# Kernel tuning notes

Measured on AMD Instinct MI355X. Metric: run time of the kernel, lower is better.

## Reference

```python
import jax, jax.numpy as jnp
import numpy as np

V, D, T, B, MS, WIN, EOS = 10000, 256, 128, 8, 4, 1, 4
S = MS + 1          # decoder segment length (y_input0 + MAX_SEGMENT tokens)
HRATE = 0.1
LOGINF = 1e6


def setup_inputs() -> dict:
    key = jax.random.key(0)
    ks = jax.random.split(key, 17)
    s = lambda i, shape: (jax.random.normal(ks[i], shape, jnp.float32) * 0.05)
    return dict(
        x_ids=jax.random.randint(ks[0], (B, T + 2 * WIN), 0, V),
        lens=jnp.full((B,), T, dtype=jnp.int32),
        emb=s(1, (V, D)),
        y_start=s(2, (1, D)),
        cell_Wi=s(3, (4 * D, D)), cell_Wh=s(4, (4 * D, D)), cell_b=s(5, (4 * D,)),
        yin0_W=s(6, (D, D)), yin0_b=s(7, (D,)),
        hlin_W=s(8, (2 * D, D)), hlin_b=s(9, (2 * D,)),
        l0_Wi=s(10, (4 * D, D)), l0_Wh=s(11, (4 * D, D)), l0_b=s(12, (4 * D,)),
        l1_Wi=s(13, (4 * D, D)), l1_Wh=s(14, (4 * D, D)), l1_b=s(15, (4 * D,)),
        out_b=s(16, (V,)),
    )


def _cell(x, h, c, Wi, Wh, b):
    # torch LSTM gate order: i, f, g, o
    g = x @ Wi.T + h @ Wh.T + b
    i, f, gg, o = jnp.split(g, 4, axis=-1)
    c2 = jax.nn.sigmoid(f) * c + jax.nn.sigmoid(i) * jnp.tanh(gg)
    return jax.nn.sigmoid(o) * jnp.tanh(c2), c2


def reference(x_ids, lens, emb, y_start, cell_Wi, cell_Wh, cell_b,
              yin0_W, yin0_b, hlin_W, hlin_b,
              l0_Wi, l0_Wh, l0_b, l1_Wi, l1_Wh, l1_b, out_b):
    y = x_ids[:, WIN:-WIN]                     # [B, T] target ids
    x = emb[y]                                 # [B, T, D]

    # --- encoder LSTMCell scan over j_start (state persists across schedule) ---
    seq = jnp.concatenate(
        [jnp.broadcast_to(y_start, (B, D))[None], jnp.transpose(x, (1, 0, 2))[:-1]], 0)  # [T,B,D]
    z = jnp.zeros((B, D), x.dtype)
    def enc_step(carry, xt):
        h, c = carry
        h2, c2 = _cell(xt, h, c, cell_Wi, cell_Wh, cell_b)
        return (h2, c2), h2
    _, h_seq = jax.lax.scan(enc_step, (z, z), seq)        # [T, B, D]

    drop_h = HRATE * h_seq
    y_in0 = drop_h @ yin0_W.T + yin0_b                    # [T, B, D]
    h0_all = jnp.tanh(drop_h @ hlin_W.T + hlin_b).reshape(T, B, 2, D)  # per-layer init h

    # --- build decoder inputs [T, B, S, D]: (y_input0, x[j_start:j_start+MS]) ---
    xp = jnp.pad(x, ((0, 0), (0, MS), (0, 0)))            # zero-pad time (causal => pads don't affect valid outputs)
    pos = jnp.arange(T)[:, None] + jnp.arange(MS)[None, :]           # [T, MS]
    seg_x = jnp.transpose(xp[:, pos], (1, 0, 2, 3))       # [T, B, MS, D]
    seg = jnp.concatenate([y_in0[:, :, None, :], seg_x], axis=2)     # [T, B, S, D]

    # --- 2-layer LSTM decoder, vmapped over j_start ---
    def decode(seg_t, h_init):                            # seg_t [B,S,D], h_init [B,2,D]
        def step(carry, xt):
            (h0, c0), (h1, c1) = carry
            h0n, c0n = _cell(xt, h0, c0, l0_Wi, l0_Wh, l0_b)
            h1n, c1n = _cell(h0n, h1, c1, l1_Wi, l1_Wh, l1_b)
            return ((h0n, c0n), (h1n, c1n)), h1n
        init = ((h_init[:, 0], z), (h_init[:, 1], z))
        _, hs = jax.lax.scan(step, init, jnp.transpose(seg_t, (1, 0, 2)))
        return jnp.transpose(hs, (1, 0, 2))               # [B, S, D]
    dec_h = jax.vmap(decode)(seg, h0_all)                 # [T, B, S, D]

    # --- tied output projection + log-softmax (only needed gathers kept) ---
    logits = jnp.einsum('tbsd,vd->tbsv', dec_h, emb) + out_b         # [T,B,S,V]
    logZ = jax.nn.logsumexp(logits, axis=-1)                          # [T,B,S]

    tgt = jnp.transpose(y[:, jnp.clip(pos, 0, T - 1)], (1, 0, 2))     # [T,B,MS]
    tgt_lp = jnp.take_along_axis(logits[:, :, :MS, :], tgt[..., None], axis=3)[..., 0] \
             - logZ[:, :, :MS]                                        # [T,B,MS]
    pmask = (pos < T)[:, None, :]
    cum = jnp.cumsum(jnp.where(pmask, tgt_lp, 0.0), axis=2)           # [T,B,MS]
    eos_lp = logits[:, :, 1:, EOS] - logZ[:, :, 1:]                   # [T,B,MS]

    kmask = (jnp.arange(T)[:, None] + jnp.arange(1, MS + 1)[None, :]) <= T   # [T,MS]
    body = jnp.where(kmask[:, None, :], cum + eos_lp, -LOGINF)        # [T,B,MS]
    logpy = jnp.concatenate([jnp.full((T, 1, B), -LOGINF, body.dtype),
                             jnp.transpose(body, (0, 2, 1))], axis=1)  # [T, MS+1, B]

    # --- alpha forward DP: alpha[j] = logsumexp_L alpha[j-L] + logpy[j-L][L] ---
    jj = jnp.arange(1, T + 1)[:, None]
    ii = jnp.arange(MS)[None, :]
    sstart = jj - MS + ii                                             # [T,MS]
    LPG = jnp.where((sstart >= 0)[..., None],
                    logpy[jnp.clip(sstart, 0), jnp.broadcast_to(MS - ii, (T, MS))],
                    -LOGINF)                                          # [T,MS,B]

    Apad0 = jnp.full((MS + T + 1, B), -LOGINF, logpy.dtype).at[MS].set(0.0)
    def dp_step(Apad, args):
        j, lpg = args
        win = jax.lax.dynamic_slice(Apad, (j, 0), (MS, B))            # alpha[j-MS .. j-1]
        aj = jax.nn.logsumexp(win + lpg, axis=0)
        return jax.lax.dynamic_update_slice(Apad, aj[None], (MS + j, 0)), None
    Apad, _ = jax.lax.scan(dp_step, Apad0, (jnp.arange(1, T + 1), LPG))
    alpha = Apad[MS:]                                                 # [T+1, B]

    ret = -jnp.sum(alpha[lens, jnp.arange(B)]) / jnp.sum(lens).astype(alpha.dtype)
    return ret
```

## Files before the change

### kernel.cpp

```cpp
#include <hip/hip_runtime.h>

#define V_ 10000
#define D_ 256
#define T_ 128
#define B_ 8
#define MS_ 4
#define S_ 5
#define EOS_ 4

typedef unsigned short b16_t;
typedef __attribute__((ext_vector_type(8))) short s16x8;
typedef __attribute__((ext_vector_type(8))) unsigned short u16x8;
typedef __attribute__((ext_vector_type(4))) float f32x4;
typedef __attribute__((ext_vector_type(2))) _Float16 h16x2;

__device__ inline b16_t f2bf(float f) {
  union { float f; unsigned u; } v; v.f = f;
  unsigned r = v.u + 0x7FFFu + ((v.u >> 16) & 1u);
  return (b16_t)(r >> 16);
}
__device__ inline float bf2f(b16_t h) {
  union { unsigned u; float f; } v; v.u = ((unsigned)h) << 16; return v.f;
}
__device__ inline float sigm_(float x) { return 1.0f / (1.0f + __expf(-x)); }
__device__ inline float tanh_(float x) { return 2.0f / (1.0f + __expf(-2.0f * x)) - 1.0f; }
__device__ inline h16x2 bch(unsigned u) { return __builtin_bit_cast(h16x2, u); }
__device__ inline unsigned pkh(float a, float b) {
  h16x2 v; v.x = (_Float16)a; v.y = (_Float16)b;
  return __builtin_bit_cast(unsigned, v);
}

#if __has_builtin(__builtin_amdgcn_fdot2)
#define FDOT2(a, b, c) __builtin_amdgcn_fdot2((a), (b), (c), false)
#else
#define FDOT2(a, b, c) ((c) + (float)(a).x * (float)(b).x + (float)(a).y * (float)(b).y)
#endif

__device__ inline void cvt4(const float* __restrict__ s, b16_t* __restrict__ d) {
  float4 v = *(const float4*)s;
  ushort4 o = { f2bf(v.x), f2bf(v.y), f2bf(v.z), f2bf(v.w) };
  *(ushort4*)d = o;
}

__global__ void k_prep(const float* __restrict__ emb, const float* __restrict__ cWi,
                       const float* __restrict__ y0W, const float* __restrict__ hlW,
                       const float* __restrict__ l0Wi, const float* __restrict__ l0Wh,
                       const float* __restrict__ l1Wi, const float* __restrict__ l1Wh,
                       const float* __restrict__ cWh, const int* __restrict__ x_ids,
                       const float* __restrict__ y_st,
                       b16_t* __restrict__ emb_bf, b16_t* __restrict__ cWi_bf,
                       b16_t* __restrict__ y0W_bf, b16_t* __restrict__ hlW_bf,
                       b16_t* __restrict__ l0Wi_bf, b16_t* __restrict__ l0Wh_bf,
                       b16_t* __restrict__ Wcat_bf, unsigned* __restrict__ Whf,
                       b16_t* __restrict__ seq_bf, b16_t* __restrict__ seg_bf) {
  for (long i = (long)blockIdx.x * blockDim.x + threadIdx.x; i < 1410048L;
       i += (long)gridDim.x * blockDim.x) {
    if (i < 640000L) { cvt4(emb + i * 4, emb_bf + i * 4); }
    else if (i < 705536L) { long j = i - 640000L; cvt4(cWi + j * 4, cWi_bf + j * 4); }
    else if (i < 721920L) { long j = i - 705536L; cvt4(y0W + j * 4, y0W_bf + j * 4); }
    else if (i < 754688L) { long j = i - 721920L; cvt4(hlW + j * 4, hlW_bf + j * 4); }
    else if (i < 820224L) { long j = i - 754688L; cvt4(l0Wi + j * 4, l0Wi_bf + j * 4); }
    else if (i < 885760L) { long j = i - 820224L; cvt4(l0Wh + j * 4, l0Wh_bf + j * 4); }
    else if (i < 1016832L) {
      long j = (i - 885760L) * 4;
      long n = j >> 9; int k = (int)(j & 511);
      const float* src = (k < 256) ? (l1Wi + n * 256 + k) : (l1Wh + n * 256 + (k - 256));
      cvt4(src, Wcat_bf + j);
    } else if (i < 1082368L) {
      long j = i - 1016832L;
      float4 v = *(const float4*)(cWh + j * 4);
      Whf[2 * j] = pkh(v.x, v.y);
      Whf[2 * j + 1] = pkh(v.z, v.w);
    } else if (i < 1147904L) {
      long j = i - 1082368L;
      int m = (int)(j >> 6), c = (int)(j & 63) * 4;
      int t = m >> 3, b = m & 7;
      const float* src = (t == 0) ? (y_st + c)
                                  : (emb + (size_t)x_ids[b * (T_ + 2) + t] * D_ + c);
      cvt4(src, seq_bf + (size_t)m * D_ + c);
    } else {
      long j = i - 1147904L;
      int r = (int)(j >> 6), c = (int)(j & 63) * 4;
      int p = r >> 2, s = 1 + (r & 3);
      int t = p >> 3, b = p & 7;
      int tt = t + s - 1;
      int ps = r + (r >> 2) + 1;
      if (tt < T_) {
        int tok = x_ids[b * (T_ + 2) + tt + 1];
        cvt4(emb + (size_t)tok * D_ + c, seg_bf + (size_t)ps * 256 + c);
      } else {
        ushort4 z = {0, 0, 0, 0};
        *(ushort4*)(seg_bf + (size_t)ps * 256 + c) = z;
      }
    }
  }
}

__global__ __launch_bounds__(256) void k_gemm_big(
    const b16_t* __restrict__ seq_bf, const b16_t* __restrict__ cWi_bf,
    const float* __restrict__ cb, float* __restrict__ encX,
    const b16_t* __restrict__ seg_bf, const b16_t* __restrict__ l0Wi_bf,
    const float* __restrict__ l0b, float* __restrict__ X0) {
  __shared__ b16_t As[64][264];
  __shared__ b16_t Bs[64][264];
  int bx = blockIdx.x, by = blockIdx.y;
  const b16_t* Ab; const b16_t* Bw; const float* bias; float* C;
  int rb, remap;
  if (bx < 16) { Ab = seq_bf; Bw = cWi_bf; bias = cb; C = encX; rb = bx * 64; remap = 0; }
  else { Ab = seg_bf; Bw = l0Wi_bf; bias = l0b; C = X0; rb = (bx - 16) * 64; remap = 1; }
  int colBase = by * 64;
  int tid = threadIdx.x;
  for (int i = tid; i < 64 * 32; i += 256) {
    int r = i >> 5, c = (i & 31) * 8;
    int rr = rb + r;
    int ar = remap ? (rr + (rr >> 2) + 1) : rr;
    *(u16x8*)&As[r][c] = *(const u16x8*)(Ab + (size_t)ar * 256 + c);
    *(u16x8*)&Bs[r][c] = *(const u16x8*)(Bw + (size_t)(colBase + r) * 256 + c);
  }
  __syncthreads();
  int w = tid >> 6, l = tid & 63, lr = l & 15, kg = l >> 4;
  f32x4 acc[4] = {{0.f,0.f,0.f,0.f},{0.f,0.f,0.f,0.f},{0.f,0.f,0.f,0.f},{0.f,0.f,0.f,0.f}};
  for (int kk = 0; kk < 8; ++kk) {
    s16x8 a = *(const s16x8*)&As[w * 16 + lr][kk * 32 + kg * 8];
#pragma unroll
    for (int f = 0; f < 4; ++f) {
      s16x8 b = *(const s16x8*)&Bs[f * 16 + lr][kk * 32 + kg * 8];
      acc[f] = __builtin_amdgcn_mfma_f32_16x16x32_bf16(a, b, acc[f], 0, 0, 0);
    }
  }
#pragma unroll
  for (int f = 0; f < 4; ++f) {
#pragma unroll
    for (int r = 0; r < 4; ++r) {
      int mm = rb + w * 16 + kg * 4 + r;
      int cr = remap ? (mm + (mm >> 2) + 1) : mm;
      int n = colBase + f * 16 + lr;
      C[(size_t)cr * 1024 + n] = acc[f][r] + bias[n];
    }
  }
}

__global__ __launch_bounds__(512) __attribute__((amdgpu_waves_per_eu(2, 2)))
void k_encoder(const unsigned* __restrict__ Whf, const float* __restrict__ encX,
               b16_t* __restrict__ droph) {
  __shared__ uint4 wtail[16][512];
  __shared__ unsigned hbuf[128];
  __shared__ float gl[1024];
  int batch = blockIdx.x;
  int tid = threadIdx.x;
  int r0 = tid, r1 = tid + 512;
  unsigned wa[96], wb[96];
  {
    const uint4* p0 = (const uint4*)(Whf + (size_t)r0 * 128);
    const uint4* p1 = (const uint4*)(Whf + (size_t)r1 * 128);
#pragma unroll
    for (int i = 0; i < 24; ++i) {
      uint4 v = p0[i];
      wa[4*i] = v.x; wa[4*i+1] = v.y; wa[4*i+2] = v.z; wa[4*i+3] = v.w;
    }
#pragma unroll
    for (int i = 0; i < 24; ++i) {
      uint4 v = p1[i];
      wb[4*i] = v.x; wb[4*i+1] = v.y; wb[4*i+2] = v.z; wb[4*i+3] = v.w;
    }
#pragma unroll
    for (int i = 0; i < 8; ++i) wtail[i][tid] = p0[24 + i];
#pragma unroll
    for (int i = 0; i < 8; ++i) wtail[8 + i][tid] = p1[24 + i];
  }
#pragma unroll
  for (int i = 0; i < 96; ++i) asm volatile("v_mov_b32 %0, %0" : "+v"(wa[i]));
#pragma unroll
  for (int i = 0; i < 96; ++i) asm volatile("v_mov_b32 %0, %0" : "+v"(wb[i]));
  if (tid < 128) hbuf[tid] = 0;
  float c = 0.f;
  float a0n = encX[((size_t)0 * 8 + batch) * 1024 + r0];
  float a1n = encX[((size_t)0 * 8 + batch) * 1024 + r1];
  __syncthreads();
#pragma unroll 1
  for (int t = 0; t < 128; ++t) {
    float a0 = a0n, a1 = a1n;
    if (t < 127) {
      a0n = encX[((size_t)(t + 1) * 8 + batch) * 1024 + r0];
      a1n = encX[((size_t)(t + 1) * 8 + batch) * 1024 + r1];
    }
    float s0 = 0.f, s1 = 0.f, s2 = 0.f, s3 = 0.f;
#pragma unroll
    for (int j = 0; j < 24; ++j) {
      uint4 hv = *(const uint4*)&hbuf[4 * j];
      s0 = FDOT2(bch(hv.x), bch(wa[4*j+0]), s0);
      s0 = FDOT2(bch(hv.y), bch(wa[4*j+1]), s0);
      s1 = FDOT2(bch(hv.z), bch(wa[4*j+2]), s1);
      s1 = FDOT2(bch(hv.w), bch(wa[4*j+3]), s1);
      s2 = FDOT2(bch(hv.x), bch(wb[4*j+0]), s2);
      s2 = FDOT2(bch(hv.y), bch(wb[4*j+1]), s2);
      s3 = FDOT2(bch(hv.z), bch(wb[4*j+2]), s3);
      s3 = FDOT2(bch(hv.w), bch(wb[4*j+3]), s3);
    }
#pragma unroll
    for (int j = 0; j < 8; ++j) {
      uint4 hv = *(const uint4*)&hbuf[96 + 4 * j];
      uint4 w0 = wtail[j][tid];
      uint4 w1 = wtail[8 + j][tid];
      s0 = FDOT2(bch(hv.x), bch(w0.x), s0);
      s0 = FDOT2(bch(hv.y), bch(w0.y), s0);
      s1 = FDOT2(bch(hv.z), bch(w0.z), s1);
      s1 = FDOT2(bch(hv.w), bch(w0.w), s1);
      s2 = FDOT2(bch(hv.x), bch(w1.x), s2);
      s2 = FDOT2(bch(hv.y), bch(w1.y), s2);
      s3 = FDOT2(bch(hv.z), bch(w1.z), s3);
      s3 = FDOT2(bch(hv.w), bch(w1.w), s3);
    }
    gl[r0] = a0 + s0 + s1;
    gl[r1] = a1 + s2 + s3;
    __syncthreads();
    if (tid < 256) {
      float gi = gl[tid],       gf = gl[256 + tid];
      float gg = gl[512 + tid], go = gl[768 + tid];
      float c2 = sigm_(gf) * c + sigm_(gi) * tanh_(gg);
      float h2 = sigm_(go) * tanh_(c2);
      c = c2;
      droph[((size_t)t * 8 + batch) * 256 + tid] = f2bf(0.1f * h2);
      ((_Float16*)hbuf)[tid] = (_Float16)h2;
    }
    __syncthreads();
  }
}

__global__ __launch_bounds__(256) void k_proj(
    const b16_t* __restrict__ droph, const b16_t* __restrict__ y0W_bf,
    const float* __restrict__ y0b, const b16_t* __restrict__ hlW_bf,
    const float* __restrict__ hlb, b16_t* __restrict__ seg_bf,
    b16_t* __restrict__ hcat) {
  __shared__ b16_t As[64][264];
  __shared__ b16_t Bs[64][264];
  int bx = blockIdx.x, by = blockIdx.y;
  const b16_t* Bw; const float* bias; int colBase, mode;
  if (by < 4) { Bw = y0W_bf; bias = y0b; colBase = by * 64; mode = 0; }
  else { Bw = hlW_bf; bias = hlb; colBase = (by - 4) * 64; mode = 1; }
  int rowBase = bx * 64;
  int tid = threadIdx.x;
  for (int i = tid; i < 64 * 32; i += 256) {
    int r = i >> 5, c = (i & 31) * 8;
    *(u16x8*)&As[r][c] = *(const u16x8*)(droph + (size_t)(rowBase + r) * 256 + c);
    *(u16x8*)&Bs[r][c] = *(const u16x8*)(Bw + (size_t)(colBase + r) * 256 + c);
  }
  __syncthreads();
  int w = tid >> 6, l = tid & 63, lr = l & 15, kg = l >> 4;
  f32x4 acc[4] = {{0.f,0.f,0.f,0.f},{0.f,0.f,0.f,0.f},{0.f,0.f,0.f,0.f},{0.f,0.f,0.f,0.f}};
  for (int kk = 0; kk < 8; ++kk) {
    s16x8 a = *(const s16x8*)&As[w * 16 + lr][kk * 32 + kg * 8];
#pragma unroll
    for (int f = 0; f < 4; ++f) {
      s16x8 b = *(const s16x8*)&Bs[f * 16 + lr][kk * 32 + kg * 8];
      acc[f] = __builtin_amdgcn_mfma_f32_16x16x32_bf16(a, b, acc[f], 0, 0, 0);
    }
  }
#pragma unroll
  for (int f = 0; f < 4; ++f) {
#pragma unroll
    for (int r = 0; r < 4; ++r) {
      int m = rowBase + w * 16 + kg * 4 + r;
      int n = colBase + f * 16 + lr;
      float v = acc[f][r] + bias[n];
      if (mode == 0) seg_bf[(size_t)m * 1280 + n] = f2bf(v);
      else hcat[(size_t)m * 512 + n] = f2bf(tanh_(v));
    }
  }
}

__global__ __launch_bounds__(256) void k_gemm(const b16_t* __restrict__ A, int lda,
                                              const b16_t* __restrict__ Bw,
                                              const float* __restrict__ bias,
                                              float* __restrict__ C, int ldc) {
  __shared__ b16_t As[64][264];
  __shared__ b16_t Bs[64][264];
  int tid = threadIdx.x;
  int rowBase = blockIdx.x * 64, colBase = blockIdx.y * 64;
  for (int i = tid; i < 64 * 32; i += 256) {
    int r = i >> 5, c = (i & 31) * 8;
    *(u16x8*)&As[r][c] = *(const u16x8*)(A + (size_t)(rowBase + r) * lda + c);
    *(u16x8*)&Bs[r][c] = *(const u16x8*)(Bw + (size_t)(colBase + r) * 256 + c);
  }
  __syncthreads();
  int w = tid >> 6, l = tid & 63, lr = l & 15, kg = l >> 4;
  f32x4 acc[4] = {{0.f,0.f,0.f,0.f},{0.f,0.f,0.f,0.f},{0.f,0.f,0.f,0.f},{0.f,0.f,0.f,0.f}};
  for (int kk = 0; kk < 8; ++kk) {
    s16x8 a = *(const s16x8*)&As[w * 16 + lr][kk * 32 + kg * 8];
#pragma unroll
    for (int f = 0; f < 4; ++f) {
      s16x8 b = *(const s16x8*)&Bs[f * 16 + lr][kk * 32 + kg * 8];
      acc[f] = __builtin_amdgcn_mfma_f32_16x16x32_bf16(a, b, acc[f], 0, 0, 0);
    }
  }
#pragma unroll
  for (int f = 0; f < 4; ++f) {
#pragma unroll
    for (int r = 0; r < 4; ++r) {
      int m = rowBase + w * 16 + kg * 4 + r;
      int n = colBase + f * 16 + lr;
      C[(size_t)m * ldc + n] = acc[f][r] + bias[n];
    }
  }
}

__global__ __launch_bounds__(512) void k_dec2(
    b16_t* __restrict__ hcat,
    const b16_t* __restrict__ l0Wh_bf,
    const b16_t* __restrict__ Wcat_bf,
    const float* __restrict__ X0,
    const float* __restrict__ l1b,
    float* __restrict__ c0, float* __restrict__ c1,
    b16_t* __restrict__ dec_out, int s) {
  __shared__ b16_t A0s[16][264];
  __shared__ b16_t A1s[16][520];
  int tid = threadIdx.x;
  int R0 = blockIdx.x * 16;
  for (int i = tid; i < 16 * 32; i += 512) {
    int r = i >> 5, cc = (i & 31) * 8;
    *(u16x8*)&A0s[r][cc] = *(const u16x8*)(hcat + (size_t)(R0 + r) * 512 + cc);
    *(u16x8*)&A1s[r][256 + cc] = *(const u16x8*)(hcat + (size_t)(R0 + r) * 512 + 256 + cc);
  }
  __syncthreads();
  int w = tid >> 6, l = tid & 63, lr = l & 15, kg = l >> 4;
  {
    s16x8 af[8];
#pragma unroll
    for (int kk = 0; kk < 8; ++kk)
      af[kk] = *(const s16x8*)&A0s[lr][kk * 32 + kg * 8];
    f32x4 acc[4][2];
#pragma unroll
    for (int g = 0; g < 4; ++g)
#pragma unroll
      for (int ct = 0; ct < 2; ++ct) acc[g][ct] = f32x4{0.f, 0.f, 0.f, 0.f};
#pragma unroll
    for (int g = 0; g < 4; ++g)
#pragma unroll
      for (int ct = 0; ct < 2; ++ct) {
        int n = g * 256 + w * 32 + ct * 16 + lr;
        const b16_t* bp = l0Wh_bf + (size_t)n * 256 + kg * 8;
#pragma unroll
        for (int kk = 0; kk < 8; ++kk)
          acc[g][ct] = __builtin_amdgcn_mfma_f32_16x16x32_bf16(
              af[kk], *(const s16x8*)(bp + kk * 32), acc[g][ct], 0, 0, 0);
      }
#pragma unroll
    for (int ct = 0; ct < 2; ++ct)
#pragma unroll
      for (int r = 0; r < 4; ++r) {
        int row = kg * 4 + r, p = R0 + row, d = w * 32 + ct * 16 + lr;
        const float* xp = X0 + ((size_t)p * 5 + s) * 1024;
        float gi = acc[0][ct][r] + xp[d],       gf = acc[1][ct][r] + xp[256 + d];
        float gg = acc[2][ct][r] + xp[512 + d], go = acc[3][ct][r] + xp[768 + d];
        float cc0 = c0[(size_t)p * 256 + d];
        float c2 = sigm_(gf) * cc0 + sigm_(gi) * tanh_(gg);
        float h2 = sigm_(go) * tanh_(c2);
        c0[(size_t)p * 256 + d] = c2;
        b16_t hb = f2bf(h2);
        A1s[row][d] = hb;
        hcat[(size_t)p * 512 + d] = hb;
      }
  }
  __syncthreads();
  {
    s16x8 a1[16];
#pragma unroll
    for (int kk = 0; kk < 16; ++kk)
      a1[kk] = *(const s16x8*)&A1s[lr][kk * 32 + kg * 8];
    f32x4 acc[4][2];
#pragma unroll
    for (int g = 0; g < 4; ++g)
#pragma unroll
      for (int ct = 0; ct < 2; ++ct) acc[g][ct] = f32x4{0.f, 0.f, 0.f, 0.f};
#pragma unroll
    for (int g = 0; g < 4; ++g)
#pragma unroll
      for (int ct = 0; ct < 2; ++ct) {
        int n = g * 256 + w * 32 + ct * 16 + lr;
        const b16_t* bp = Wcat_bf + (size_t)n * 512 + kg * 8;
#pragma unroll
        for (int kk = 0; kk < 16; ++kk)
          acc[g][ct] = __builtin_amdgcn_mfma_f32_16x16x32_bf16(
              a1[kk], *(const s16x8*)(bp + kk * 32), acc[g][ct], 0, 0, 0);
      }
#pragma unroll
    for (int ct = 0; ct < 2; ++ct)
#pragma unroll
      for (int r = 0; r < 4; ++r) {
        int row = kg * 4 + r, p = R0 + row, d = w * 32 + ct * 16 + lr;
        float gi = acc[0][ct][r] + l1b[d],       gf = acc[1][ct][r] + l1b[256 + d];
        float gg = acc[2][ct][r] + l1b[512 + d], go = acc[3][ct][r] + l1b[768 + d];
        float cc1 = c1[(size_t)p * 256 + d];
        float c2 = sigm_(gf) * cc1 + sigm_(gi) * tanh_(gg);
        float h2 = sigm_(go) * tanh_(c2);
        c1[(size_t)p * 256 + d] = c2;
        b16_t hb = f2bf(h2);
        hcat[(size_t)p * 512 + 256 + d] = hb;
        dec_out[((size_t)p * 5 + s) * 256 + d] = hb;
      }
  }
}

__global__ __launch_bounds__(512) void k_logits(const b16_t* __restrict__ Abf,
                                                const b16_t* __restrict__ emb_bf,
                                                const float* __restrict__ out_b,
                                                float* __restrict__ sumexp) {
  __shared__ b16_t Bs[64][264];
  int tid = threadIdx.x;
  int rowBase = blockIdx.x * 128;
  int w = tid >> 6, l = tid & 63, lr = l & 15, kg = l >> 4;
  s16x8 af[8];
  {
    const b16_t* arow = Abf + (size_t)(rowBase + w * 16 + lr) * 256;
#pragma unroll
    for (int kk = 0; kk < 8; ++kk) af[kk] = *(const s16x8*)(arow + kk * 32 + kg * 8);
  }
  float runsum[4] = {0.f, 0.f, 0.f, 0.f};
  int t0 = blockIdx.y * 12, t1 = (t0 + 12 < 157) ? (t0 + 12) : 157;
  for (int tile = t0; tile < t1; ++tile) {
    int colBase = tile * 64;
    __syncthreads();
    for (int i = tid; i < 64 * 32; i += 512) {
      int r = i >> 5, cc = (i & 31) * 8;
      int vrow = colBase + r;
      u16x8 bv = {0, 0, 0, 0, 0, 0, 0, 0};
      if (vrow < V_) bv = *(const u16x8*)(emb_bf + (size_t)vrow * D_ + cc);
      *(u16x8*)&Bs[r][cc] = bv;
    }
    __syncthreads();
    f32x4 acc[4] = {{0.f,0.f,0.f,0.f},{0.f,0.f,0.f,0.f},{0.f,0.f,0.f,0.f},{0.f,0.f,0.f,0.f}};
#pragma unroll
    for (int kk = 0; kk < 8; ++kk) {
#pragma unroll
      for (int f = 0; f < 4; ++f) {
        s16x8 b = *(const s16x8*)&Bs[f * 16 + lr][kk * 32 + kg * 8];
        acc[f] = __builtin_amdgcn_mfma_f32_16x16x32_bf16(af[kk], b, acc[f], 0, 0, 0);
      }
    }
#pragma unroll
    for (int f = 0; f < 4; ++f) {
      int n = colBase + f * 16 + lr;
      if (n < V_) {
        float ob = out_b[n];
#pragma unroll
        for (int r = 0; r < 4; ++r) runsum[r] += __expf(acc[f][r] + ob);
      }
    }
  }
#pragma unroll
  for (int r = 0; r < 4; ++r) {
    float rs = runsum[r];
    rs += __shfl_xor(rs, 1, 64);
    rs += __shfl_xor(rs, 2, 64);
    rs += __shfl_xor(rs, 4, 64);
    rs += __shfl_xor(rs, 8, 64);
    if (lr == 0) atomicAdd(&sumexp[rowBase + w * 16 + kg * 4 + r], rs);
  }
}

__global__ void k_extract(const b16_t* __restrict__ dec_h, const b16_t* __restrict__ emb_bf,
                          const float* __restrict__ out_b, const int* __restrict__ x_ids,
                          float* __restrict__ tl, float* __restrict__ el) {
  int p = blockIdx.x, lane = threadIdx.x;
  int t = p >> 3, b = p & 7;
  for (int s = 0; s < S_; ++s) {
    const b16_t* hr = dec_h + ((size_t)p * S_ + s) * D_;
    float hv[4];
#pragma unroll
    for (int j = 0; j < 4; ++j) hv[j] = bf2f(hr[lane * 4 + j]);
    if (s < MS_) {
      int pos = t + s; if (pos > T_ - 1) pos = T_ - 1;
      int tok = x_ids[b * (T_ + 2) + pos + 1];
      const b16_t* er = emb_bf + (size_t)tok * D_;
      float ps = 0.f;
#pragma unroll
      for (int j = 0; j < 4; ++j) ps += hv[j] * bf2f(er[lane * 4 + j]);
      for (int m = 1; m < 64; m <<= 1) ps += __shfl_xor(ps, m, 64);
      if (lane == 0) tl[p * MS_ + s] = ps + out_b[tok];
    }
    if (s >= 1) {
      const b16_t* er = emb_bf + (size_t)EOS_ * D_;
      float ps = 0.f;
#pragma unroll
      for (int j = 0; j < 4; ++j) ps += hv[j] * bf2f(er[lane * 4 + j]);
      for (int m = 1; m < 64; m <<= 1) ps += __shfl_xor(ps, m, 64);
      if (lane == 0) el[p * MS_ + (s - 1)] = ps + out_b[EOS_];
    }
  }
}

__global__ __launch_bounds__(256) void k_final(const float* __restrict__ sumexp,
                                               const float* __restrict__ tl,
                                               const float* __restrict__ el,
                                               const int* __restrict__ lens,
                                               float* __restrict__ out) {
  __shared__ float logpy[T_][S_][B_];
  __shared__ float alpha[T_ + 1][B_];
  int tid = threadIdx.x;
  for (int p = tid; p < T_ * B_; p += 256) {
    int t = p >> 3, b = p & 7;
    float lz[S_];
#pragma unroll
    for (int s = 0; s < S_; ++s) lz[s] = __logf(sumexp[p * S_ + s]);
    float cum = 0.f, cums[MS_];
#pragma unroll
    for (int s = 0; s < MS_; ++s) {
      float tlp = tl[p * MS_ + s] - lz[s];
      if (t + s < T_) cum += tlp;
      cums[s] = cum;
    }
#pragma unroll
    for (int k = 1; k <= MS_; ++k) {
      float bv = -1000000.0f;
      if (t + k <= T_) bv = cums[k - 1] + (el[p * MS_ + (k - 1)] - lz[k]);
      logpy[t][k][b] = bv;
    }
  }
  __syncthreads();
  if (tid < B_) {
    int b = tid;
    alpha[0][b] = 0.f;
    for (int j = 1; j <= T_; ++j) {
      float vs[MS_], vmax = -1e30f;
#pragma unroll
      for (int k = 1; k <= MS_; ++k) {
        float vv = -2000000.0f;
        if (j - k >= 0) vv = alpha[j - k][b] + logpy[j - k][k][b];
        vs[k - 1] = vv;
        if (vv > vmax) vmax = vv;
      }
      float ssum = 0.f;
#pragma unroll
      for (int k = 0; k < MS_; ++k) ssum += __expf(vs[k] - vmax);
      alpha[j][b] = vmax + __logf(ssum);
    }
  }
  __syncthreads();
  if (tid == 0) {
    float num = 0.f, den = 0.f;
    for (int b = 0; b < B_; ++b) { num += alpha[lens[b]][b]; den += (float)lens[b]; }
    out[0] = -num / den;
  }
}

extern "C" void kernel_launch(void* const* d_in, const int* in_sizes, int n_in,
                              void* d_out, int out_size, void* d_ws, size_t ws_size,
                              hipStream_t stream) {
  const int* x_ids   = (const int*)d_in[0];
  const int* lens    = (const int*)d_in[1];
  const float* emb   = (const float*)d_in[2];
  const float* y_st  = (const float*)d_in[3];
  const float* cWi   = (const float*)d_in[4];
  const float* cWh   = (const float*)d_in[5];
  const float* cb    = (const float*)d_in[6];
  const float* y0W   = (const float*)d_in[7];
  const float* y0b   = (const float*)d_in[8];
  const float* hlW   = (const float*)d_in[9];
  const float* hlb   = (const float*)d_in[10];
  const float* l0Wi  = (const float*)d_in[11];
  const float* l0Wh  = (const float*)d_in[12];
  const float* l0b   = (const float*)d_in[13];
  const float* l1Wi  = (const float*)d_in[14];
  const float* l1Wh  = (const float*)d_in[15];
  const float* l1b   = (const float*)d_in[16];
  const float* outb  = (const float*)d_in[17];
  float* out = (float*)d_out;
  (void)in_sizes; (void)n_in; (void)out_size; (void)ws_size;

  char* ws = (char*)d_ws;
  size_t cur = 0;
  auto alloc = [&](size_t bytes) { size_t o = cur; cur += (bytes + 255) & ~(size_t)255; return o; };
  b16_t* emb_bf    = (b16_t*)(ws + alloc((size_t)V_ * D_ * 2));
  b16_t* cWi_bf    = (b16_t*)(ws + alloc(1024 * 256 * 2));
  b16_t* y0W_bf    = (b16_t*)(ws + alloc(256 * 256 * 2));
  b16_t* hlW_bf    = (b16_t*)(ws + alloc(512 * 256 * 2));
  b16_t* l0Wi_bf   = (b16_t*)(ws + alloc(1024 * 256 * 2));
  b16_t* l0Wh_bf   = (b16_t*)(ws + alloc(1024 * 256 * 2));
  b16_t* Wcat_bf   = (b16_t*)(ws + alloc(1024 * 512 * 2));
  unsigned* Whf    = (unsigned*)(ws + alloc(1024 * 128 * 4));
  b16_t* seq_bf    = (b16_t*)(ws + alloc(1024 * 256 * 2));
  float* encX      = (float*)(ws + alloc((size_t)1024 * 1024 * 4));
  b16_t* droph_bf  = (b16_t*)(ws + alloc(1024 * 256 * 2));
  b16_t* hcat      = (b16_t*)(ws + alloc(1024 * 512 * 2));
  b16_t* seg_bf    = (b16_t*)(ws + alloc((size_t)5120 * 256 * 2));
  float* X0        = (float*)(ws + alloc((size_t)5120 * 1024 * 4));
  float* c0        = (float*)(ws + alloc((size_t)2 * 1024 * 256 * 4));
  float* c1        = c0 + 1024 * 256;
  b16_t* dec_h_bf  = (b16_t*)(ws + alloc((size_t)5120 * 256 * 2));
  float* sumexp    = (float*)(ws + alloc(5120 * 4));
  float* tl        = (float*)(ws + alloc(1024 * MS_ * 4));
  float* el        = (float*)(ws + alloc(1024 * MS_ * 4));

  hipMemsetAsync(sumexp, 0, 5120 * 4, stream);
  hipMemsetAsync(c0, 0, (size_t)2 * 1024 * 256 * 4, stream);

  k_prep<<<1024, 256, 0, stream>>>(emb, cWi, y0W, hlW, l0Wi, l0Wh, l1Wi, l1Wh, cWh,
                                   x_ids, y_st,
                                   emb_bf, cWi_bf, y0W_bf, hlW_bf, l0Wi_bf, l0Wh_bf,
                                   Wcat_bf, Whf, seq_bf, seg_bf);

  k_gemm_big<<<dim3(80, 16), 256, 0, stream>>>(seq_bf, cWi_bf, cb, encX,
                                               seg_bf, l0Wi_bf, l0b, X0);
  k_encoder<<<8, 512, 0, stream>>>(Whf, encX, droph_bf);

  k_proj<<<dim3(16, 12), 256, 0, stream>>>(droph_bf, y0W_bf, y0b, hlW_bf, hlb,
                                           seg_bf, hcat);
  k_gemm<<<dim3(16, 16), 256, 0, stream>>>(seg_bf, 1280, l0Wi_bf, l0b, X0, 5120);

  for (int s = 0; s < S_; ++s)
    k_dec2<<<64, 512, 0, stream>>>(hcat, l0Wh_bf, Wcat_bf, X0, l1b, c0, c1, dec_h_bf, s);

  k_logits<<<dim3(40, 14), 512, 0, stream>>>(dec_h_bf, emb_bf, outb, sumexp);
  k_extract<<<1024, 64, 0, stream>>>(dec_h_bf, emb_bf, outb, x_ids, tl, el);
  k_final<<<1, 256, 0, stream>>>(sumexp, tl, el, lens, out);
}
```

Measured before the change: 657.3 us.

## Fuse decoder steps into one kernel and restructure encoder recurrent matvec

The five per-step decoder launches become one kernel that loops over segment positions. Cell states are kept in registers and hidden states in shared memory instead of round-tripping through global memory, which also removes the cell-state memset. The encoder recurrence is rewritten so each group of four lanes splits one row's K dimension, reducing partial sums with DPP quad swaps. All weights are held in VGPRs and AGPRs, with the h buffer padded per quarter to avoid LDS bank conflicts. This removes launch overhead and global state traffic, at the cost of high register pressure and extra cross-lane shuffles in the serial encoder loop.

```diff
diff --git a/kernel.cpp b/kernel.cpp
--- a/kernel.cpp
+++ b/kernel.cpp
@@ -35,6 +35,15 @@
 #else
 #define FDOT2(a, b, c) ((c) + (float)(a).x * (float)(b).x + (float)(a).y * (float)(b).y)
 #endif
+
+__device__ inline float qswap1(float x) {
+  return __builtin_bit_cast(float, __builtin_amdgcn_update_dpp(
+      0, __builtin_bit_cast(int, x), 0xB1, 0xF, 0xF, true));
+}
+__device__ inline float qswap2(float x) {
+  return __builtin_bit_cast(float, __builtin_amdgcn_update_dpp(
+      0, __builtin_bit_cast(int, x), 0x4E, 0xF, 0xF, true));
+}
 
 __device__ inline void cvt4(const float* __restrict__ s, b16_t* __restrict__ d) {
   float4 v = *(const float4*)s;
@@ -140,88 +149,92 @@
   }
 }
 
-__global__ __launch_bounds__(512) __attribute__((amdgpu_waves_per_eu(2, 2)))
-void k_encoder(const unsigned* __restrict__ Whf, const float* __restrict__ encX,
-               b16_t* __restrict__ droph) {
-  __shared__ uint4 wtail[16][512];
-  __shared__ unsigned hbuf[128];
+__global__ __launch_bounds__(512, 2) void k_encoder(
+    const unsigned* __restrict__ Whf, const float* __restrict__ encX,
+    b16_t* __restrict__ droph) {
+  __shared__ unsigned hbuf[144];
   __shared__ float gl[1024];
   int batch = blockIdx.x;
   int tid = threadIdx.x;
-  int r0 = tid, r1 = tid + 512;
-  unsigned wa[96], wb[96];
-  {
-    const uint4* p0 = (const uint4*)(Whf + (size_t)r0 * 128);
-    const uint4* p1 = (const uint4*)(Whf + (size_t)r1 * 128);
-#pragma unroll
-    for (int i = 0; i < 24; ++i) {
-      uint4 v = p0[i];
-      wa[4*i] = v.x; wa[4*i+1] = v.y; wa[4*i+2] = v.z; wa[4*i+3] = v.w;
-    }
-#pragma unroll
-    for (int i = 0; i < 24; ++i) {
-      uint4 v = p1[i];
-      wb[4*i] = v.x; wb[4*i+1] = v.y; wb[4*i+2] = v.z; wb[4*i+3] = v.w;
-    }
-#pragma unroll
-    for (int i = 0; i < 8; ++i) wtail[i][tid] = p0[24 + i];
-#pragma unroll
-    for (int i = 0; i < 8; ++i) wtail[8 + i][tid] = p1[24 + i];
-  }
-#pragma unroll
-  for (int i = 0; i < 96; ++i) asm volatile("v_mov_b32 %0, %0" : "+v"(wa[i]));
-#pragma unroll
-  for (int i = 0; i < 96; ++i) asm volatile("v_mov_b32 %0, %0" : "+v"(wb[i]));
-  if (tid < 128) hbuf[tid] = 0;
+  int lane = tid & 63;
+  int q = lane & 3;
+  int slot = (tid >> 6) * 16 + (lane >> 2);
+  int r0 = slot * 8;
+  unsigned wv_[160], wa_[96];
+#pragma unroll
+  for (int j = 0; j < 5; ++j) {
+    const uint4* p = (const uint4*)(Whf + (size_t)(r0 + j) * 128 + q * 32);
+#pragma unroll
+    for (int i = 0; i < 8; ++i) {
+      uint4 v = p[i];
+      wv_[j*32+4*i] = v.x; wv_[j*32+4*i+1] = v.y; wv_[j*32+4*i+2] = v.z; wv_[j*32+4*i+3] = v.w;
+    }
+  }
+#pragma unroll
+  for (int j = 0; j < 3; ++j) {
+    const uint4* p = (const uint4*)(Whf + (size_t)(r0 + 5 + j) * 128 + q * 32);
+#pragma unroll
+    for (int i = 0; i < 8; ++i) {
+      uint4 v = p[i];
+      wa_[j*32+4*i] = v.x; wa_[j*32+4*i+1] = v.y; wa_[j*32+4*i+2] = v.z; wa_[j*32+4*i+3] = v.w;
+    }
+  }
+#pragma unroll
+  for (int i = 0; i < 160; ++i) asm volatile("" : "+v"(wv_[i]));
+#pragma unroll
+  for (int i = 0; i < 96; ++i) asm volatile("" : "+a"(wa_[i]));
+  if (tid < 144) hbuf[tid] = 0;
   float c = 0.f;
-  float a0n = encX[((size_t)0 * 8 + batch) * 1024 + r0];
-  float a1n = encX[((size_t)0 * 8 + batch) * 1024 + r1];
+  float exa = encX[(size_t)batch * 1024 + r0 + q];
+  float exb = encX[(size_t)batch * 1024 + r0 + 4 + q];
   __syncthreads();
 #pragma unroll 1
   for (int t = 0; t < 128; ++t) {
-    float a0 = a0n, a1 = a1n;
+    uint4 hv[8];
+    const uint4* hp = (const uint4*)&hbuf[q * 36];
+#pragma unroll
+    for (int i = 0; i < 8; ++i) hv[i] = hp[i];
+    float p[8];
+#pragma unroll
+    for (int j = 0; j < 8; ++j) {
+      float s0 = 0.f, s1 = 0.f;
+#pragma unroll
+      for (int i = 0; i < 8; ++i) {
+        unsigned w0, w1, w2, w3;
+        if (j < 5) {
+          w0 = wv_[j*32+4*i]; w1 = wv_[j*32+4*i+1];
+          w2 = wv_[j*32+4*i+2]; w3 = wv_[j*32+4*i+3];
+        } else {
+          w0 = wa_[(j-5)*32+4*i]; w1 = wa_[(j-5)*32+4*i+1];
+          w2 = wa_[(j-5)*32+4*i+2]; w3 = wa_[(j-5)*32+4*i+3];
+        }
+        s0 = FDOT2(bch(hv[i].x), bch(w0), s0);
+        s1 = FDOT2(bch(hv[i].y), bch(w1), s1);
+        s0 = FDOT2(bch(hv[i].z), bch(w2), s0);
+        s1 = FDOT2(bch(hv[i].w), bch(w3), s1);
+      }
+      float tt = s0 + s1;
+      tt += qswap1(tt);
+      tt += qswap2(tt);
+      p[j] = tt;
+    }
+    float va = (q == 0) ? p[0] : (q == 1) ? p[1] : (q == 2) ? p[2] : p[3];
+    float vb = (q == 0) ? p[4] : (q == 1) ? p[5] : (q == 2) ? p[6] : p[7];
+    gl[r0 + q] = va + exa;
+    gl[r0 + 4 + q] = vb + exb;
     if (t < 127) {
-      a0n = encX[((size_t)(t + 1) * 8 + batch) * 1024 + r0];
-      a1n = encX[((size_t)(t + 1) * 8 + batch) * 1024 + r1];
-    }
-    float s0 = 0.f, s1 = 0.f, s2 = 0.f, s3 = 0.f;
-#pragma unroll
-    for (int j = 0; j < 24; ++j) {
-      uint4 hv = *(const uint4*)&hbuf[4 * j];
-      s0 = FDOT2(bch(hv.x), bch(wa[4*j+0]), s0);
-      s0 = FDOT2(bch(hv.y), bch(wa[4*j+1]), s0);
-      s1 = FDOT2(bch(hv.z), bch(wa[4*j+2]), s1);
-      s1 = FDOT2(bch(hv.w), bch(wa[4*j+3]), s1);
-      s2 = FDOT2(bch(hv.x), bch(wb[4*j+0]), s2);
-      s2 = FDOT2(bch(hv.y), bch(wb[4*j+1]), s2);
-      s3 = FDOT2(bch(hv.z), bch(wb[4*j+2]), s3);
-      s3 = FDOT2(bch(hv.w), bch(wb[4*j+3]), s3);
-    }
-#pragma unroll
-    for (int j = 0; j < 8; ++j) {
-      uint4 hv = *(const uint4*)&hbuf[96 + 4 * j];
-      uint4 w0 = wtail[j][tid];
-      uint4 w1 = wtail[8 + j][tid];
-      s0 = FDOT2(bch(hv.x), bch(w0.x), s0);
-      s0 = FDOT2(bch(hv.y), bch(w0.y), s0);
-      s1 = FDOT2(bch(hv.z), bch(w0.z), s1);
-      s1 = FDOT2(bch(hv.w), bch(w0.w), s1);
-      s2 = FDOT2(bch(hv.x), bch(w1.x), s2);
-      s2 = FDOT2(bch(hv.y), bch(w1.y), s2);
-      s3 = FDOT2(bch(hv.z), bch(w1.z), s3);
-      s3 = FDOT2(bch(hv.w), bch(w1.w), s3);
-    }
-    gl[r0] = a0 + s0 + s1;
-    gl[r1] = a1 + s2 + s3;
+      exa = encX[((size_t)(t + 1) * 8 + batch) * 1024 + r0 + q];
+      exb = encX[((size_t)(t + 1) * 8 + batch) * 1024 + r0 + 4 + q];
+    }
     __syncthreads();
     if (tid < 256) {
-      float gi = gl[tid],       gf = gl[256 + tid];
-      float gg = gl[512 + tid], go = gl[768 + tid];
+      int d = tid;
+      float gi = gl[d], gf = gl[256 + d], gg = gl[512 + d], go = gl[768 + d];
       float c2 = sigm_(gf) * c + sigm_(gi) * tanh_(gg);
       float h2 = sigm_(go) * tanh_(c2);
       c = c2;
-      droph[((size_t)t * 8 + batch) * 256 + tid] = f2bf(0.1f * h2);
-      ((_Float16*)hbuf)[tid] = (_Float16)h2;
+      droph[((size_t)t * 8 + batch) * 256 + d] = f2bf(0.1f * h2);
+      ((_Float16*)hbuf)[(d >> 6) * 72 + (d & 63)] = (_Float16)h2;
     }
     __syncthreads();
   }
@@ -304,14 +317,13 @@
   }
 }
 
-__global__ __launch_bounds__(512) void k_dec2(
-    b16_t* __restrict__ hcat,
+__global__ __launch_bounds__(512) void k_dec5(
+    const b16_t* __restrict__ hcat,
     const b16_t* __restrict__ l0Wh_bf,
     const b16_t* __restrict__ Wcat_bf,
     const float* __restrict__ X0,
     const float* __restrict__ l1b,
-    float* __restrict__ c0, float* __restrict__ c1,
-    b16_t* __restrict__ dec_out, int s) {
+    b16_t* __restrict__ dec_out) {
   __shared__ b16_t A0s[16][264];
   __shared__ b16_t A1s[16][520];
   int tid = threadIdx.x;
@@ -321,83 +333,90 @@
     *(u16x8*)&A0s[r][cc] = *(const u16x8*)(hcat + (size_t)(R0 + r) * 512 + cc);
     *(u16x8*)&A1s[r][256 + cc] = *(const u16x8*)(hcat + (size_t)(R0 + r) * 512 + 256 + cc);
   }
+  int w = tid >> 6, l = tid & 63, lr = l & 15, kg = l >> 4;
+  float c0st[2][4] = {{0,0,0,0},{0,0,0,0}};
+  float c1st[2][4] = {{0,0,0,0},{0,0,0,0}};
   __syncthreads();
-  int w = tid >> 6, l = tid & 63, lr = l & 15, kg = l >> 4;
-  {
+#pragma unroll 1
+  for (int s = 0; s < S_; ++s) {
     s16x8 af[8];
 #pragma unroll
     for (int kk = 0; kk < 8; ++kk)
       af[kk] = *(const s16x8*)&A0s[lr][kk * 32 + kg * 8];
-    f32x4 acc[4][2];
-#pragma unroll
-    for (int g = 0; g < 4; ++g)
-#pragma unroll
-      for (int ct = 0; ct < 2; ++ct) acc[g][ct] = f32x4{0.f, 0.f, 0.f, 0.f};
-#pragma unroll
-    for (int g = 0; g < 4; ++g)
-#pragma unroll
-      for (int ct = 0; ct < 2; ++ct) {
-        int n = g * 256 + w * 32 + ct * 16 + lr;
-        const b16_t* bp = l0Wh_bf + (size_t)n * 256 + kg * 8;
-#pragma unroll
-        for (int kk = 0; kk < 8; ++kk)
-          acc[g][ct] = __builtin_amdgcn_mfma_f32_16x16x32_bf16(
-              af[kk], *(const s16x8*)(bp + kk * 32), acc[g][ct], 0, 0, 0);
-      }
-#pragma unroll
-    for (int ct = 0; ct < 2; ++ct)
-#pragma unroll
-      for (int r = 0; r < 4; ++r) {
-        int row = kg * 4 + r, p = R0 + row, d = w * 32 + ct * 16 + lr;
-        const float* xp = X0 + ((size_t)p * 5 + s) * 1024;
-        float gi = acc[0][ct][r] + xp[d],       gf = acc[1][ct][r] + xp[256 + d];
-        float gg = acc[2][ct][r] + xp[512 + d], go = acc[3][ct][r] + xp[768 + d];
-        float cc0 = c0[(size_t)p * 256 + d];
-        float c2 = sigm_(gf) * cc0 + sigm_(gi) * tanh_(gg);
-        float h2 = sigm_(go) * tanh_(c2);
-        c0[(size_t)p * 256 + d] = c2;
-        b16_t hb = f2bf(h2);
-        A1s[row][d] = hb;
-        hcat[(size_t)p * 512 + d] = hb;
-      }
-  }
-  __syncthreads();
-  {
+    __syncthreads();
+    {
+      f32x4 acc[4][2];
+#pragma unroll
+      for (int g = 0; g < 4; ++g)
+#pragma unroll
+        for (int ct = 0; ct < 2; ++ct) acc[g][ct] = f32x4{0.f, 0.f, 0.f, 0.f};
+#pragma unroll
+      for (int g = 0; g < 4; ++g)
+#pragma unroll
+        for (int ct = 0; ct < 2; ++ct) {
+          int n = g * 256 + w * 32 + ct * 16 + lr;
+          const b16_t* bp = l0Wh_bf + (size_t)n * 256 + kg * 8;
+#pragma unroll
+          for (int kk = 0; kk < 8; ++kk)
+            acc[g][ct] = __builtin_amdgcn_mfma_f32_16x16x32_bf16(
+                af[kk], *(const s16x8*)(bp + kk * 32), acc[g][ct], 0, 0, 0);
+        }
+#pragma unroll
+      for (int ct = 0; ct < 2; ++ct)
+#pragma unroll
+        for (int r = 0; r < 4; ++r) {
+          int row = kg * 4 + r, p = R0 + row, d = w * 32 + ct * 16 + lr;
+          const float* xp = X0 + ((size_t)p * 5 + s) * 1024;
+          float gi = acc[0][ct][r] + xp[d],       gf = acc[1][ct][r] + xp[256 + d];
+          float gg = acc[2][ct][r] + xp[512 + d], go = acc[3][ct][r] + xp[768 + d];
+          float cc0 = c0st[ct][r];
+          float c2 = sigm_(gf) * cc0 + sigm_(gi) * tanh_(gg);
+          float h2 = sigm_(go) * tanh_(c2);
+          c0st[ct][r] = c2;
+          b16_t hb = f2bf(h2);
+          A1s[row][d] = hb;
+          A0s[row][d] = hb;
+        }
+    }
+    __syncthreads();
     s16x8 a1[16];
 #pragma unroll
     for (int kk = 0; kk < 16; ++kk)
       a1[kk] = *(const s16x8*)&A1s[lr][kk * 32 + kg * 8];
-    f32x4 acc[4][2];
-#pragma unroll
-    for (int g = 0; g < 4; ++g)
-#pragma unroll
-      for (int ct = 0; ct < 2; ++ct) acc[g][ct] = f32x4{0.f, 0.f, 0.f, 0.f};
-#pragma unroll
-    for (int g = 0; g < 4; ++g)
-#pragma unroll
-      for (int ct = 0; ct < 2; ++ct) {
-        int n = g * 256 + w * 32 + ct * 16 + lr;
-        const b16_t* bp = Wcat_bf + (size_t)n * 512 + kg * 8;
-#pragma unroll
-        for (int kk = 0; kk < 16; ++kk)
-          acc[g][ct] = __builtin_amdgcn_mfma_f32_16x16x32_bf16(
-              a1[kk], *(const s16x8*)(bp + kk * 32), acc[g][ct], 0, 0, 0);
-      }
-#pragma unroll
-    for (int ct = 0; ct < 2; ++ct)
-#pragma unroll
-      for (int r = 0; r < 4; ++r) {
-        int row = kg * 4 + r, p = R0 + row, d = w * 32 + ct * 16 + lr;
-        float gi = acc[0][ct][r] + l1b[d],       gf = acc[1][ct][r] + l1b[256 + d];
-        float gg = acc[2][ct][r] + l1b[512 + d], go = acc[3][ct][r] + l1b[768 + d];
-        float cc1 = c1[(size_t)p * 256 + d];
-        float c2 = sigm_(gf) * cc1 + sigm_(gi) * tanh_(gg);
-        float h2 = sigm_(go) * tanh_(c2);
-        c1[(size_t)p * 256 + d] = c2;
-        b16_t hb = f2bf(h2);
-        hcat[(size_t)p * 512 + 256 + d] = hb;
-        dec_out[((size_t)p * 5 + s) * 256 + d] = hb;
-      }
+    __syncthreads();
+    {
+      f32x4 acc[4][2];
+#pragma unroll
+      for (int g = 0; g < 4; ++g)
+#pragma unroll
+        for (int ct = 0; ct < 2; ++ct) acc[g][ct] = f32x4{0.f, 0.f, 0.f, 0.f};
+#pragma unroll
+      for (int g = 0; g < 4; ++g)
+#pragma unroll
+        for (int ct = 0; ct < 2; ++ct) {
+          int n = g * 256 + w * 32 + ct * 16 + lr;
+          const b16_t* bp = Wcat_bf + (size_t)n * 512 + kg * 8;
+#pragma unroll
+          for (int kk = 0; kk < 16; ++kk)
+            acc[g][ct] = __builtin_amdgcn_mfma_f32_16x16x32_bf16(
+                a1[kk], *(const s16x8*)(bp + kk * 32), acc[g][ct], 0, 0, 0);
+        }
+#pragma unroll
+      for (int ct = 0; ct < 2; ++ct)
+#pragma unroll
+        for (int r = 0; r < 4; ++r) {
+          int row = kg * 4 + r, p = R0 + row, d = w * 32 + ct * 16 + lr;
+          float gi = acc[0][ct][r] + l1b[d],       gf = acc[1][ct][r] + l1b[256 + d];
+          float gg = acc[2][ct][r] + l1b[512 + d], go = acc[3][ct][r] + l1b[768 + d];
+          float cc1 = c1st[ct][r];
+          float c2 = sigm_(gf) * cc1 + sigm_(gi) * tanh_(gg);
+          float h2 = sigm_(go) * tanh_(c2);
+          c1st[ct][r] = c2;
+          b16_t hb = f2bf(h2);
+          A1s[row][256 + d] = hb;
+          dec_out[((size_t)p * 5 + s) * 256 + d] = hb;
+        }
+    }
   }
 }
 
@@ -584,15 +603,12 @@
   b16_t* hcat      = (b16_t*)(ws + alloc(1024 * 512 * 2));
   b16_t* seg_bf    = (b16_t*)(ws + alloc((size_t)5120 * 256 * 2));
   float* X0        = (float*)(ws + alloc((size_t)5120 * 1024 * 4));
-  float* c0        = (float*)(ws + alloc((size_t)2 * 1024 * 256 * 4));
-  float* c1        = c0 + 1024 * 256;
   b16_t* dec_h_bf  = (b16_t*)(ws + alloc((size_t)5120 * 256 * 2));
   float* sumexp    = (float*)(ws + alloc(5120 * 4));
   float* tl        = (float*)(ws + alloc(1024 * MS_ * 4));
   float* el        = (float*)(ws + alloc(1024 * MS_ * 4));
 
   hipMemsetAsync(sumexp, 0, 5120 * 4, stream);
-  hipMemsetAsync(c0, 0, (size_t)2 * 1024 * 256 * 4, stream);
 
   k_prep<<<1024, 256, 0, stream>>>(emb, cWi, y0W, hlW, l0Wi, l0Wh, l1Wi, l1Wh, cWh,
                                    x_ids, y_st,
@@ -607,8 +623,7 @@
                                            seg_bf, hcat);
   k_gemm<<<dim3(16, 16), 256, 0, stream>>>(seg_bf, 1280, l0Wi_bf, l0b, X0, 5120);
 
-  for (int s = 0; s < S_; ++s)
-    k_dec2<<<64, 512, 0, stream>>>(hcat, l0Wh_bf, Wcat_bf, X0, l1b, c0, c1, dec_h_bf, s);
+  k_dec5<<<64, 512, 0, stream>>>(hcat, l0Wh_bf, Wcat_bf, X0, l1b, dec_h_bf);
 
   k_logits<<<dim3(40, 14), 512, 0, stream>>>(dec_h_bf, emb_bf, outb, sumexp);
   k_extract<<<1024, 64, 0, stream>>>(dec_h_bf, emb_bf, outb, x_ids, tl, el);
```

After: 791.8 us. 1.2x slower.

## Split encoder LSTM across four blocks per batch with global flag sync

Applied to the files above, without the earlier changes.

The recurrent encoder now runs on 32 blocks instead of 8. Each batch row is split across 4 blocks, and each block owns 64 hidden units, so all of its weights fit in registers and no LDS tail is needed. Hidden-state slices are exchanged every timestep through global memory, with per-step flags and spin-waiting replacing the single-block LDS exchange. This shortens each step's matvec but adds inter-block communication latency on the serial critical path, and it relies on all 32 blocks being co-resident.

```diff
diff --git a/kernel.cpp b/kernel.cpp
--- a/kernel.cpp
+++ b/kernel.cpp
@@ -35,6 +35,11 @@
 #else
 #define FDOT2(a, b, c) ((c) + (float)(a).x * (float)(b).x + (float)(a).y * (float)(b).y)
 #endif
+
+__device__ inline float qswap1(float x) {
+  return __builtin_bit_cast(float, __builtin_amdgcn_update_dpp(
+      0, __builtin_bit_cast(int, x), 0xB1, 0xF, 0xF, true));
+}
 
 __device__ inline void cvt4(const float* __restrict__ s, b16_t* __restrict__ d) {
   float4 v = *(const float4*)s;
@@ -140,90 +145,87 @@
   }
 }
 
-__global__ __launch_bounds__(512) __attribute__((amdgpu_waves_per_eu(2, 2)))
-void k_encoder(const unsigned* __restrict__ Whf, const float* __restrict__ encX,
-               b16_t* __restrict__ droph) {
-  __shared__ uint4 wtail[16][512];
+__global__ __launch_bounds__(512, 2) void k_encoder(
+    const unsigned* __restrict__ Whf,
+    const float* __restrict__ encX,
+    unsigned* __restrict__ hglob,
+    int* __restrict__ flags,
+    b16_t* __restrict__ droph) {
   __shared__ unsigned hbuf[128];
-  __shared__ float gl[1024];
-  int batch = blockIdx.x;
+  __shared__ float gl[256];
+  int b = blockIdx.x & 7, q = blockIdx.x >> 3;
   int tid = threadIdx.x;
-  int r0 = tid, r1 = tid + 512;
-  unsigned wa[96], wb[96];
+  int r = tid >> 1, ch = tid & 1;
+  int growr = ((r >> 6) << 8) + q * 64 + (r & 63);
+  unsigned wv[64];
   {
-    const uint4* p0 = (const uint4*)(Whf + (size_t)r0 * 128);
-    const uint4* p1 = (const uint4*)(Whf + (size_t)r1 * 128);
-#pragma unroll
-    for (int i = 0; i < 24; ++i) {
-      uint4 v = p0[i];
-      wa[4*i] = v.x; wa[4*i+1] = v.y; wa[4*i+2] = v.z; wa[4*i+3] = v.w;
-    }
-#pragma unroll
-    for (int i = 0; i < 24; ++i) {
-      uint4 v = p1[i];
-      wb[4*i] = v.x; wb[4*i+1] = v.y; wb[4*i+2] = v.z; wb[4*i+3] = v.w;
-    }
-#pragma unroll
-    for (int i = 0; i < 8; ++i) wtail[i][tid] = p0[24 + i];
-#pragma unroll
-    for (int i = 0; i < 8; ++i) wtail[8 + i][tid] = p1[24 + i];
-  }
-#pragma unroll
-  for (int i = 0; i < 96; ++i) asm volatile("v_mov_b32 %0, %0" : "+v"(wa[i]));
-#pragma unroll
-  for (int i = 0; i < 96; ++i) asm volatile("v_mov_b32 %0, %0" : "+v"(wb[i]));
+    const uint4* wp = (const uint4*)(Whf + (size_t)growr * 128 + ch * 64);
+#pragma unroll
+    for (int i = 0; i < 16; ++i) {
+      uint4 v = wp[i];
+      wv[4*i] = v.x; wv[4*i+1] = v.y; wv[4*i+2] = v.z; wv[4*i+3] = v.w;
+    }
+  }
+#pragma unroll
+  for (int i = 0; i < 64; ++i) asm volatile("" : "+v"(wv[i]));
   if (tid < 128) hbuf[tid] = 0;
   float c = 0.f;
-  float a0n = encX[((size_t)0 * 8 + batch) * 1024 + r0];
-  float a1n = encX[((size_t)0 * 8 + batch) * 1024 + r1];
+  float ex = encX[(size_t)b * 1024 + growr];
   __syncthreads();
 #pragma unroll 1
   for (int t = 0; t < 128; ++t) {
-    float a0 = a0n, a1 = a1n;
-    if (t < 127) {
-      a0n = encX[((size_t)(t + 1) * 8 + batch) * 1024 + r0];
-      a1n = encX[((size_t)(t + 1) * 8 + batch) * 1024 + r1];
-    }
-    float s0 = 0.f, s1 = 0.f, s2 = 0.f, s3 = 0.f;
-#pragma unroll
-    for (int j = 0; j < 24; ++j) {
-      uint4 hv = *(const uint4*)&hbuf[4 * j];
-      s0 = FDOT2(bch(hv.x), bch(wa[4*j+0]), s0);
-      s0 = FDOT2(bch(hv.y), bch(wa[4*j+1]), s0);
-      s1 = FDOT2(bch(hv.z), bch(wa[4*j+2]), s1);
-      s1 = FDOT2(bch(hv.w), bch(wa[4*j+3]), s1);
-      s2 = FDOT2(bch(hv.x), bch(wb[4*j+0]), s2);
-      s2 = FDOT2(bch(hv.y), bch(wb[4*j+1]), s2);
-      s3 = FDOT2(bch(hv.z), bch(wb[4*j+2]), s3);
-      s3 = FDOT2(bch(hv.w), bch(wb[4*j+3]), s3);
-    }
-#pragma unroll
-    for (int j = 0; j < 8; ++j) {
-      uint4 hv = *(const uint4*)&hbuf[96 + 4 * j];
-      uint4 w0 = wtail[j][tid];
-      uint4 w1 = wtail[8 + j][tid];
-      s0 = FDOT2(bch(hv.x), bch(w0.x), s0);
-      s0 = FDOT2(bch(hv.y), bch(w0.y), s0);
-      s1 = FDOT2(bch(hv.z), bch(w0.z), s1);
-      s1 = FDOT2(bch(hv.w), bch(w0.w), s1);
-      s2 = FDOT2(bch(hv.x), bch(w1.x), s2);
-      s2 = FDOT2(bch(hv.y), bch(w1.y), s2);
-      s3 = FDOT2(bch(hv.z), bch(w1.z), s3);
-      s3 = FDOT2(bch(hv.w), bch(w1.w), s3);
-    }
-    gl[r0] = a0 + s0 + s1;
-    gl[r1] = a1 + s2 + s3;
+    float s0 = 0.f, s1 = 0.f;
+    const uint4* hp = (const uint4*)&hbuf[ch * 64];
+#pragma unroll 4
+    for (int i = 0; i < 16; ++i) {
+      uint4 hv = hp[i];
+      s0 = FDOT2(bch(hv.x), bch(wv[4*i+0]), s0);
+      s1 = FDOT2(bch(hv.y), bch(wv[4*i+1]), s1);
+      s0 = FDOT2(bch(hv.z), bch(wv[4*i+2]), s0);
+      s1 = FDOT2(bch(hv.w), bch(wv[4*i+3]), s1);
+    }
+    float sum = s0 + s1;
+    sum += qswap1(sum);
+    if (ch == 0) gl[r] = sum + ex;
     __syncthreads();
-    if (tid < 256) {
-      float gi = gl[tid],       gf = gl[256 + tid];
-      float gg = gl[512 + tid], go = gl[768 + tid];
+    if (tid < 64) {
+      float gi = gl[tid], gf = gl[64 + tid], gg = gl[128 + tid], go = gl[192 + tid];
       float c2 = sigm_(gf) * c + sigm_(gi) * tanh_(gg);
       float h2 = sigm_(go) * tanh_(c2);
       c = c2;
-      droph[((size_t)t * 8 + batch) * 256 + tid] = f2bf(0.1f * h2);
-      ((_Float16*)hbuf)[tid] = (_Float16)h2;
-    }
-    __syncthreads();
+      droph[((size_t)t * 8 + b) * 256 + q * 64 + tid] = f2bf(0.1f * h2);
+      float hnb = qswap1(h2);
+      if ((tid & 1) == 0) {
+        unsigned pk = pkh(h2, hnb);
+        hbuf[q * 32 + (tid >> 1)] = pk;
+        if (t < 127)
+          __hip_atomic_store(&hglob[((((size_t)(t + 1) * 8 + b) * 4 + q) * 32) + (tid >> 1)],
+                             pk, __ATOMIC_RELAXED, __HIP_MEMORY_SCOPE_AGENT);
+      }
+    }
+    if (t < 127) {
+      if (tid == 0) {
+        asm volatile("s_waitcnt vmcnt(0)" ::: "memory");
+        __hip_atomic_store(&flags[((t + 1) * 8 + b) * 4 + q], 1,
+                           __ATOMIC_RELAXED, __HIP_MEMORY_SCOPE_AGENT);
+      }
+      if (tid >= 64 && tid < 160) {
+        int idx = tid - 64;
+        int ro = idx >> 5;
+        int rq = ro + (ro >= q);
+        int dw = idx & 31;
+        int* fp = &flags[((t + 1) * 8 + b) * 4 + rq];
+        while (!__hip_atomic_load(fp, __ATOMIC_RELAXED, __HIP_MEMORY_SCOPE_AGENT))
+          __builtin_amdgcn_s_sleep(1);
+        asm volatile("" ::: "memory");
+        unsigned v = __hip_atomic_load(
+            &hglob[((((size_t)(t + 1) * 8 + b) * 4 + rq) * 32) + dw],
+            __ATOMIC_RELAXED, __HIP_MEMORY_SCOPE_AGENT);
+        hbuf[rq * 32 + dw] = v;
+      }
+      ex = encX[((size_t)(t + 1) * 8 + b) * 1024 + growr];
+      __syncthreads();
+    }
   }
 }
 
@@ -588,10 +590,12 @@
   float* c1        = c0 + 1024 * 256;
   b16_t* dec_h_bf  = (b16_t*)(ws + alloc((size_t)5120 * 256 * 2));
   float* sumexp    = (float*)(ws + alloc(5120 * 4));
+  int* flags       = (int*)(ws + alloc(129 * 8 * 4 * 4));
+  unsigned* hglob  = (unsigned*)(ws + alloc((size_t)129 * 8 * 4 * 32 * 4));
   float* tl        = (float*)(ws + alloc(1024 * MS_ * 4));
   float* el        = (float*)(ws + alloc(1024 * MS_ * 4));
 
-  hipMemsetAsync(sumexp, 0, 5120 * 4, stream);
+  hipMemsetAsync(sumexp, 0, 20480 + 16512, stream);
   hipMemsetAsync(c0, 0, (size_t)2 * 1024 * 256 * 4, stream);
 
   k_prep<<<1024, 256, 0, stream>>>(emb, cWi, y0W, hlW, l0Wi, l0Wh, l1Wi, l1Wh, cWh,
@@ -601,7 +605,7 @@
 
   k_gemm_big<<<dim3(80, 16), 256, 0, stream>>>(seq_bf, cWi_bf, cb, encX,
                                                seg_bf, l0Wi_bf, l0b, X0);
-  k_encoder<<<8, 512, 0, stream>>>(Whf, encX, droph_bf);
+  k_encoder<<<32, 512, 0, stream>>>(Whf, encX, hglob, flags, droph_bf);
 
   k_proj<<<dim3(16, 12), 256, 0, stream>>>(droph_bf, y0W_bf, y0b, hlW_bf, hlb,
                                            seg_bf, hcat);
```

Measured after the change: 1.037 ms. 57.8% more time.
